# Performance work log

Hardware: AMD Instinct MI355X
Metric: run time of the kernel (lower is better)

Reference implementation:

```python
import jax, jax.numpy as jnp
import numpy as np

EPS = 1e-5
LEAKY = 0.2


def _wn(v, g):
    # weight norm over all dims except output-channel dim 0 (torch default dim=0)
    return g * v / jnp.sqrt(jnp.sum(v * v, axis=(1, 2), keepdims=True))


def _conv1d(x_bsc, w, b):
    # x_bsc: [B,S,C_in]; w: [C_out,C_in,3]; kernel 3, stride 1, pad 1
    x = x_bsc.transpose(0, 2, 1)  # NCH
    y = jax.lax.conv_general_dilated(x, w, (1,), [(1, 1)],
                                     dimension_numbers=("NCH", "OIH", "NCH"))
    y = y + b[None, :, None]
    return y.transpose(0, 2, 1)


def _adain(x, style, lengths, proj_w, proj_b):
    # masked per-(sample,channel) instance norm over valid length, then style affine, then mask
    B, S, H = x.shape
    hs = style @ proj_w.T + proj_b            # [B, 2H]
    gamma, beta = hs[:, :H], hs[:, H:]
    mask = (jnp.arange(S)[None, :] < lengths[:, None]).astype(x.dtype)[..., None]  # [B,S,1]
    cnt = lengths.astype(x.dtype)[:, None, None]
    mean = jnp.sum(x * mask, axis=1, keepdims=True) / cnt
    var = jnp.sum(jnp.square(x - mean) * mask, axis=1, keepdims=True) / cnt  # biased, as F.instance_norm
    xn = (x - mean) * jax.lax.rsqrt(var + EPS)
    out = ((1.0 + gamma[:, None, :]) * xn + beta[:, None, :]) * mask
    return out, mask


def setup_inputs() -> dict:
    key = jax.random.key(0)
    ks = jax.random.split(key, 12)
    B, S, H, STY = 8, 2048, 512, 128
    inp = {
        "hidden_states": jax.random.normal(ks[0], (B, S, H), jnp.float32),
        "style": jax.random.normal(ks[1], (B, STY), jnp.float32),
        "input_lengths": jax.random.randint(ks[2], (B,), S // 2, S + 1, jnp.int32),
        # AdaIN projections (torch Linear: [out,in])
        "proj1_w": jax.random.normal(ks[3], (2 * H, STY), jnp.float32) * 0.02,
        "proj1_b": jnp.zeros((2 * H,), jnp.float32),
        "proj2_w": jax.random.normal(ks[4], (2 * H, STY), jnp.float32) * 0.02,
        "proj2_b": jnp.zeros((2 * H,), jnp.float32),
        # weight-normed conv1 / conv2: v [out,in,3], g [out,1,1], bias [out]
        "conv1_v": jax.random.normal(ks[5], (H, H, 3), jnp.float32) * 0.02,
        "conv1_g": jnp.ones((H, 1, 1), jnp.float32),
        "conv1_b": jnp.zeros((H,), jnp.float32),
        "conv2_v": jax.random.normal(ks[6], (H, H, 3), jnp.float32) * 0.02,
        "conv2_g": jnp.ones((H, 1, 1), jnp.float32),
        "conv2_b": jnp.zeros((H,), jnp.float32),
    }
    return inp


def reference(hidden_states, style, input_lengths,
              proj1_w, proj1_b, proj2_w, proj2_b,
              conv1_v, conv1_g, conv1_b, conv2_v, conv2_g, conv2_b):
    w1 = _wn(conv1_v, conv1_g)
    w2 = _wn(conv2_v, conv2_g)
    # residual branch
    h, mask = _adain(hidden_states, style, input_lengths, proj1_w, proj1_b)
    h = jnp.where(h >= 0, h, LEAKY * h)
    h = _conv1d(h, w1, conv1_b) * mask
    h, _ = _adain(h, style, input_lengths, proj2_w, proj2_b)
    h = jnp.where(h >= 0, h, LEAKY * h)
    h = _conv1d(h, w2, conv2_b) * mask
    # shortcut is identity (no upsample, no learned shortcut)
    return (h + hidden_states) / jnp.sqrt(jnp.asarray(2.0, hidden_states.dtype))
```

## Files before the change

kernel.cpp:

```cpp
#include <hip/hip_runtime.h>

#define NB 8
#define SS 2048
#define HH 512
#define NSTY 128
#define SP (SS + 2)
#define EPSF 1e-5f

#define BM 128
#define BN 128
#define BK 64

typedef __attribute__((ext_vector_type(8))) short short8;
typedef __attribute__((ext_vector_type(4))) float floatx4;
typedef __attribute__((ext_vector_type(4))) unsigned short u16x4;
typedef unsigned short u16;

__device__ __forceinline__ float bf2f(u16 u) {
  union { float f; unsigned int i; } v; v.i = ((unsigned int)u) << 16; return v.f;
}
__device__ __forceinline__ u16 f2bf(float f) {
  union { float f; unsigned int i; } v; v.f = f;
  unsigned int x = v.i;
  return (u16)((x + 0x7fffu + ((x >> 16) & 1u)) >> 16);
}
__device__ __forceinline__ float lrelu(float v) { return v >= 0.f ? v : 0.2f * v; }

__device__ __forceinline__ void gld_lds16(const u16* g, u16* l) {
  __builtin_amdgcn_global_load_lds((const __attribute__((address_space(1))) void*)g,
                                   (__attribute__((address_space(3))) void*)l, 16, 0, 0);
}

__global__ void k_setup(const float* __restrict__ style,
                        const float* __restrict__ p1w, const float* __restrict__ p1b,
                        const float* __restrict__ p2w, const float* __restrict__ p2b,
                        const float* __restrict__ c1v, const float* __restrict__ c1g,
                        const float* __restrict__ c2v, const float* __restrict__ c2g,
                        u16* __restrict__ wt1, u16* __restrict__ wt2,
                        float* __restrict__ g1, float* __restrict__ be1,
                        float* __restrict__ g2, float* __restrict__ be2,
                        float* __restrict__ stats ) {
  int bid = blockIdx.x;
  if (bid < 2 * HH) {
    int o = bid % HH;
    int which = bid / HH;
    const float* v = which ? c2v : c1v;
    const float* g = which ? c2g : c1g;
    u16* wt = which ? wt2 : wt1;
    float s = 0.f;
    for (int e = threadIdx.x; e < HH * 3; e += 256) {
      float x = v[o * HH * 3 + e];
      s += x * x;
    }
    for (int off = 32; off > 0; off >>= 1) s += __shfl_down(s, off, 64);
    __shared__ float red[4];
    int wid = threadIdx.x >> 6, lane = threadIdx.x & 63;
    if (lane == 0) red[wid] = s;
    __syncthreads();
    float tot = red[0] + red[1] + red[2] + red[3];
    float scale = g[o] / sqrtf(tot);
    for (int e = threadIdx.x; e < HH * 3; e += 256) {
      int i = e / 3, k = e % 3;
      wt[(k * HH + o) * HH + i] = f2bf(v[o * HH * 3 + e] * scale);
    }
  } else if (bid < 2 * HH + 64) {
    int idx = (bid - 2 * HH) * 256 + threadIdx.x;
    int which = idx / (NB * 2 * HH);
    int r = idx % (NB * 2 * HH);
    int b = r / (2 * HH);
    int j = r % (2 * HH);
    const float* w = which ? p2w : p1w;
    const float* bias = which ? p2b : p1b;
    float acc = bias[j];
    const float* st = style + b * NSTY;
    const float* wr = w + j * NSTY;
    for (int t = 0; t < NSTY; t++) acc += st[t] * wr[t];
    float* gd = which ? g2 : g1;
    float* bd = which ? be2 : be1;
    if (j < HH) gd[b * HH + j] = acc;
    else        bd[b * HH + (j - HH)] = acc;
  } else {
    int i = (bid - 2 * HH - 64) * 256 + threadIdx.x;
    stats[i] = 0.f;
  }
}

#define SSPLIT1 64
__global__ void k_stats_f32(const float* __restrict__ x, const int* __restrict__ lens,
                            float* __restrict__ sum, float* __restrict__ sumsq) {
  int b = blockIdx.x & 7;
  int chunk = blockIdx.x >> 3;
  int s0 = chunk * (SS / SSPLIT1);
  int h4 = (threadIdx.x & 127) * 4;
  int sr = threadIdx.x >> 7;
  int len = lens[b];
  float4 sm = {0.f, 0.f, 0.f, 0.f}, sq = {0.f, 0.f, 0.f, 0.f};
#pragma unroll
  for (int i = 0; i < 16; i++) {
    int s = s0 + i * 2 + sr;
    float4 v = *(const float4*)(x + ((long)(b * SS + s)) * HH + h4);
    float m = (s < len) ? 1.f : 0.f;
    v.x *= m; v.y *= m; v.z *= m; v.w *= m;
    sm.x += v.x; sm.y += v.y; sm.z += v.z; sm.w += v.w;
    sq.x += v.x * v.x; sq.y += v.y * v.y; sq.z += v.z * v.z; sq.w += v.w * v.w;
  }
  atomicAdd(&sum[b * HH + h4 + 0], sm.x);
  atomicAdd(&sum[b * HH + h4 + 1], sm.y);
  atomicAdd(&sum[b * HH + h4 + 2], sm.z);
  atomicAdd(&sum[b * HH + h4 + 3], sm.w);
  atomicAdd(&sumsq[b * HH + h4 + 0], sq.x);
  atomicAdd(&sumsq[b * HH + h4 + 1], sq.y);
  atomicAdd(&sumsq[b * HH + h4 + 2], sq.z);
  atomicAdd(&sumsq[b * HH + h4 + 3], sq.w);
}

__global__ void k_prep_f32(const float* __restrict__ x,
                           const float* __restrict__ sum, const float* __restrict__ sumsq,
                           const float* __restrict__ gam, const float* __restrict__ bet,
                           const int* __restrict__ lens, u16* __restrict__ z) {
  __shared__ float a_tab[HH], c_tab[HH];
  int b = blockIdx.x & 7;
  int c = blockIdx.x >> 3;
  int len = lens[b];
  {
    float rc = 1.f / (float)len;
    int i0 = threadIdx.x * 2;
    float2 sm = *(const float2*)(sum + b * HH + i0);
    float2 sq = *(const float2*)(sumsq + b * HH + i0);
    float2 gv = *(const float2*)(gam + b * HH + i0);
    float2 bv = *(const float2*)(bet + b * HH + i0);
    float m0 = sm.x * rc, m1 = sm.y * rc;
    float a0 = (1.f + gv.x) * rsqrtf(sq.x * rc - m0 * m0 + EPSF);
    float a1 = (1.f + gv.y) * rsqrtf(sq.y * rc - m1 * m1 + EPSF);
    a_tab[i0] = a0;            a_tab[i0 + 1] = a1;
    c_tab[i0] = bv.x - m0 * a0; c_tab[i0 + 1] = bv.y - m1 * a1;
  }
  __syncthreads();
  int r = c * 2 + (threadIdx.x >> 7);
  int i = (threadIdx.x & 127) * 4;
  int s = r - 1;
  u16x4 outv;
  if (s < 0 || s >= SS || s >= len) {
    outv = (u16x4){0, 0, 0, 0};
  } else {
    const float4 xv = *(const float4*)(x + ((long)(b * SS + s)) * HH + i);
    const float4 av = *(const float4*)(&a_tab[i]);
    const float4 cv = *(const float4*)(&c_tab[i]);
    outv.x = f2bf(lrelu(av.x * xv.x + cv.x));
    outv.y = f2bf(lrelu(av.y * xv.y + cv.y));
    outv.z = f2bf(lrelu(av.z * xv.z + cv.z));
    outv.w = f2bf(lrelu(av.w * xv.w + cv.w));
  }
  *(u16x4*)(z + ((long)(b * SP + r)) * HH + i) = outv;
}

__global__ void k_prep_bf16(const u16* __restrict__ y,
                            const float* __restrict__ sum, const float* __restrict__ sumsq,
                            const float* __restrict__ gam, const float* __restrict__ bet,
                            const int* __restrict__ lens, u16* __restrict__ z) {
  __shared__ float a_tab[HH], c_tab[HH];
  int b = blockIdx.x & 7;
  int c = blockIdx.x >> 3;
  int len = lens[b];
  {
    float rc = 1.f / (float)len;
    int i0 = threadIdx.x * 2;
    float2 sm = *(const float2*)(sum + b * HH + i0);
    float2 sq = *(const float2*)(sumsq + b * HH + i0);
    float2 gv = *(const float2*)(gam + b * HH + i0);
    float2 bv = *(const float2*)(bet + b * HH + i0);
    float m0 = sm.x * rc, m1 = sm.y * rc;
    float a0 = (1.f + gv.x) * rsqrtf(sq.x * rc - m0 * m0 + EPSF);
    float a1 = (1.f + gv.y) * rsqrtf(sq.y * rc - m1 * m1 + EPSF);
    a_tab[i0] = a0;            a_tab[i0 + 1] = a1;
    c_tab[i0] = bv.x - m0 * a0; c_tab[i0 + 1] = bv.y - m1 * a1;
  }
  __syncthreads();
  int r = c * 2 + (threadIdx.x >> 7);
  int i = (threadIdx.x & 127) * 4;
  int s = r - 1;
  u16x4 outv;
  if (s < 0 || s >= SS || s >= len) {
    outv = (u16x4){0, 0, 0, 0};
  } else {
    const u16x4 yv = *(const u16x4*)(y + ((long)(b * SS + s)) * HH + i);
    const float4 av = *(const float4*)(&a_tab[i]);
    const float4 cv = *(const float4*)(&c_tab[i]);
    outv.x = f2bf(lrelu(av.x * bf2f(yv.x) + cv.x));
    outv.y = f2bf(lrelu(av.y * bf2f(yv.y) + cv.y));
    outv.z = f2bf(lrelu(av.z * bf2f(yv.z) + cv.z));
    outv.w = f2bf(lrelu(av.w * bf2f(yv.w) + cv.w));
  }
  *(u16x4*)(z + ((long)(b * SP + r)) * HH + i) = outv;
}

__global__ __launch_bounds__(512, 4) void k_conv(const u16* __restrict__ z,
                                                 const u16* __restrict__ wt,
                                                 const float* __restrict__ bias,
                                                 const int* __restrict__ lens,
                                                 u16* __restrict__ yout,
                                                 const float* __restrict__ resid,
                                                 float* __restrict__ fout,
                                                 float* __restrict__ sum,
                                                 float* __restrict__ sumsq) {
  __shared__ __align__(16) u16 L[2][2][BM * BK];

  int nwg = gridDim.x;
  int bid = blockIdx.x;
  int t = (bid & 7) * (nwg >> 3) + (bid >> 3);
  int bn0 = (t % (HH / BN)) * BN; t /= (HH / BN);
  int bm0 = (t % (SS / BM)) * BM; t /= (SS / BM);
  int b = t;

  int tid = threadIdx.x;
  int wave = tid >> 6, lane = tid & 63;
  int team = wave >> 2;
  int tw = wave & 3;
  int wr = tw >> 1, wc = tw & 1;
  int l15 = lane & 15, l4 = lane >> 4;

  int t256 = tid & 255;
  int trow = t256 >> 3;
  int tslot = t256 & 7;

  u16* LA = &L[team][0][0];
  u16* LB = &L[team][1][0];

  const u16* zb = z + (size_t)b * SP * HH;
  int len = lens[b];
  int kt0 = team * 12;

  floatx4 acc[4][4] = {};

  for (int kt = 0; kt < 12; kt++) {
    int k0 = (kt0 + kt) * BK;
    const u16* wkb = wt + (size_t)(k0 >> 9) * HH * HH + (k0 & 511);
#pragma unroll
    for (int rr = 0; rr < 4; rr++) {
      int r = rr * 32 + trow;
      int sc = (tslot ^ (r & 7)) * 8;
      gld_lds16(zb + (size_t)(bm0 + r) * HH + k0 + sc, LA + rr * 2048 + t256 * 8);
    }
#pragma unroll
    for (int rr = 0; rr < 4; rr++) {
      int r = rr * 32 + trow;
      int sc = (tslot ^ (r & 7)) * 8;
      gld_lds16(wkb + (size_t)(bn0 + r) * HH + sc, LB + rr * 2048 + t256 * 8);
    }
    __syncthreads();
#pragma unroll
    for (int kk = 0; kk < 2; kk++) {
      short8 afr[4], bfr[4];
#pragma unroll
      for (int i = 0; i < 4; i++) {
        int ar = wr * 64 + i * 16 + l15;
        afr[i] = *(const short8*)&LA[ar * BK + (((kk * 4 + l4) ^ (ar & 7)) * 8)];
      }
#pragma unroll
      for (int j = 0; j < 4; j++) {
        int br = wc * 64 + j * 16 + l15;
        bfr[j] = *(const short8*)&LB[br * BK + (((kk * 4 + l4) ^ (br & 7)) * 8)];
      }
#pragma unroll
      for (int am = 0; am < 4; am++)
#pragma unroll
        for (int bn = 0; bn < 4; bn++)
          acc[am][bn] = __builtin_amdgcn_mfma_f32_16x16x32_bf16(afr[am], bfr[bn], acc[am][bn], 0, 0, 0);
    }
    __syncthreads();
  }

  floatx4* scr = (floatx4*)&L[0][0][0];
  floatx4* my = scr + (size_t)team * 2048;
  if (team == 0) {
#pragma unroll
    for (int am = 0; am < 4; am++) {
      my[(am * 2 + 0) * 256 + t256] = acc[am][2];
      my[(am * 2 + 1) * 256 + t256] = acc[am][3];
    }
  } else {
#pragma unroll
    for (int am = 0; am < 4; am++) {
      my[(am * 2 + 0) * 256 + t256] = acc[am][0];
      my[(am * 2 + 1) * 256 + t256] = acc[am][1];
    }
  }
  __syncthreads();
  const floatx4* other = scr + (size_t)(team ^ 1) * 2048;
  if (team == 0) {
#pragma unroll
    for (int am = 0; am < 4; am++) {
      acc[am][0] += other[(am * 2 + 0) * 256 + t256];
      acc[am][1] += other[(am * 2 + 1) * 256 + t256];
    }
  } else {
#pragma unroll
    for (int am = 0; am < 4; am++) {
      acc[am][2] += other[(am * 2 + 0) * 256 + t256];
      acc[am][3] += other[(am * 2 + 1) * 256 + t256];
    }
  }

#define EPI(BN_) do {                                                        \
    int o = bn0 + wc * 64 + (BN_) * 16 + l15;                                \
    float bv = bias[o];                                                      \
    float psum = 0.f, psq = 0.f;                                             \
    _Pragma("unroll")                                                        \
    for (int am = 0; am < 4; am++) {                                         \
      _Pragma("unroll")                                                      \
      for (int r = 0; r < 4; r++) {                                          \
        int s = bm0 + wr * 64 + am * 16 + l4 * 4 + r;                        \
        float v = acc[am][BN_][r] + bv;                                      \
        v = (s < len) ? v : 0.f;                                             \
        size_t off = ((size_t)(b * SS + s)) * HH + o;                        \
        if (fout) {                                                          \
          fout[off] = (v + resid[off]) * 0.70710678118654752f;               \
        } else {                                                             \
          yout[off] = f2bf(v);                                               \
          psum += v;                                                         \
          psq += v * v;                                                      \
        }                                                                    \
      }                                                                      \
    }                                                                        \
    if (sum) {                                                               \
      psum += __shfl_xor(psum, 16, 64);                                      \
      psum += __shfl_xor(psum, 32, 64);                                      \
      psq  += __shfl_xor(psq, 16, 64);                                       \
      psq  += __shfl_xor(psq, 32, 64);                                       \
      if (l4 == 0) {                                                         \
        atomicAdd(&sum[b * HH + o], psum);                                   \
        atomicAdd(&sumsq[b * HH + o], psq);                                  \
      }                                                                      \
    }                                                                        \
  } while (0)

  if (team == 0) { EPI(0); EPI(1); }
  else           { EPI(2); EPI(3); }
#undef EPI
}

extern "C" void kernel_launch(void* const* d_in, const int* in_sizes, int n_in,
                              void* d_out, int out_size, void* d_ws, size_t ws_size,
                              hipStream_t stream) {
  const float* x    = (const float*)d_in[0];
  const float* sty  = (const float*)d_in[1];
  const int*   lens = (const int*)d_in[2];
  const float* p1w  = (const float*)d_in[3];
  const float* p1b  = (const float*)d_in[4];
  const float* p2w  = (const float*)d_in[5];
  const float* p2b  = (const float*)d_in[6];
  const float* c1v  = (const float*)d_in[7];
  const float* c1g  = (const float*)d_in[8];
  const float* c1b  = (const float*)d_in[9];
  const float* c2v  = (const float*)d_in[10];
  const float* c2g  = (const float*)d_in[11];
  const float* c2b  = (const float*)d_in[12];
  float* out = (float*)d_out;

  char* ws = (char*)d_ws;
  size_t cur = 0;
  auto alloc = [&](size_t bytes) {
    void* p = ws + cur;
    cur += (bytes + 255) & ~(size_t)255;
    return p;
  };
  u16*   wt1  = (u16*)alloc((size_t)3 * HH * HH * 2);
  u16*   wt2  = (u16*)alloc((size_t)3 * HH * HH * 2);
  float* g1   = (float*)alloc(NB * HH * 4);
  float* be1  = (float*)alloc(NB * HH * 4);
  float* g2   = (float*)alloc(NB * HH * 4);
  float* be2  = (float*)alloc(NB * HH * 4);
  float* sum1 = (float*)alloc(NB * HH * 4);
  float* sq1  = (float*)alloc(NB * HH * 4);
  float* sum2 = (float*)alloc(NB * HH * 4);
  float* sq2  = (float*)alloc(NB * HH * 4);
  u16*   z1   = (u16*)alloc((size_t)NB * SP * HH * 2);
  u16*   y1   = (u16*)alloc((size_t)NB * SS * HH * 2);
  u16*   z2   = (u16*)alloc((size_t)NB * SP * HH * 2);

  const int CGRID = NB * (SS / BM) * (HH / BN);

  k_setup<<<2 * HH + 128, 256, 0, stream>>>(sty, p1w, p1b, p2w, p2b,
                                            c1v, c1g, c2v, c2g,
                                            wt1, wt2, g1, be1, g2, be2, sum1);

  k_stats_f32<<<NB * SSPLIT1, 256, 0, stream>>>(x, lens, sum1, sq1);

  k_prep_f32<<<NB * (SP * HH / 4 / 256), 256, 0, stream>>>(x, sum1, sq1, g1, be1,
                                                           lens, z1);

  k_conv<<<CGRID, 512, 0, stream>>>(z1, wt1, c1b, lens, y1,
                                    nullptr, nullptr, sum2, sq2);

  k_prep_bf16<<<NB * (SP * HH / 4 / 256), 256, 0, stream>>>(y1, sum2, sq2, g2, be2,
                                                            lens, z2);

  k_conv<<<CGRID, 512, 0, stream>>>(z2, wt2, c2b, lens, nullptr,
                                    x, out, nullptr, nullptr);
}
```

Measured before the change: 115.3 us.

## Use producer-consumer warp specialization with double-buffered LDS in conv GEMM

Replaces the split-K scheme, where two teams of four waves each took half the K range and reduced through LDS, with warp specialization. Waves 4-7 issue global-to-LDS loads into a double buffer while waves 0-3 run MFMA on the other buffer, separated by one barrier per K tile. This removes the cross-team LDS reduction and overlaps loads with compute. The cost is that half the waves no longer do math, so per-tile MFMA throughput per block is halved.

```diff
diff --git a/kernel.cpp b/kernel.cpp
--- a/kernel.cpp
+++ b/kernel.cpp
@@ -214,52 +214,52 @@
 
   int tid = threadIdx.x;
   int wave = tid >> 6, lane = tid & 63;
-  int team = wave >> 2;
-  int tw = wave & 3;
-  int wr = tw >> 1, wc = tw & 1;
+  int wr = (wave >> 1) & 1, wc = wave & 1;
   int l15 = lane & 15, l4 = lane >> 4;
 
   int t256 = tid & 255;
   int trow = t256 >> 3;
   int tslot = t256 & 7;
 
-  u16* LA = &L[team][0][0];
-  u16* LB = &L[team][1][0];
-
   const u16* zb = z + (size_t)b * SP * HH;
   int len = lens[b];
-  int kt0 = team * 12;
 
   floatx4 acc[4][4] = {};
 
-  for (int kt = 0; kt < 12; kt++) {
-    int k0 = (kt0 + kt) * BK;
+  auto stage = [&](int buf, int kt) {
+    int k0 = kt * BK;
     const u16* wkb = wt + (size_t)(k0 >> 9) * HH * HH + (k0 & 511);
+    u16* dA = &L[buf][0][0];
+    u16* dB = &L[buf][1][0];
 #pragma unroll
     for (int rr = 0; rr < 4; rr++) {
       int r = rr * 32 + trow;
       int sc = (tslot ^ (r & 7)) * 8;
-      gld_lds16(zb + (size_t)(bm0 + r) * HH + k0 + sc, LA + rr * 2048 + t256 * 8);
+      gld_lds16(zb + (size_t)(bm0 + r) * HH + k0 + sc, dA + rr * 2048 + t256 * 8);
     }
 #pragma unroll
     for (int rr = 0; rr < 4; rr++) {
       int r = rr * 32 + trow;
       int sc = (tslot ^ (r & 7)) * 8;
-      gld_lds16(wkb + (size_t)(bn0 + r) * HH + sc, LB + rr * 2048 + t256 * 8);
-    }
-    __syncthreads();
+      gld_lds16(wkb + (size_t)(bn0 + r) * HH + sc, dB + rr * 2048 + t256 * 8);
+    }
+  };
+
+  auto compute = [&](int buf) {
+    const u16* sA = &L[buf][0][0];
+    const u16* sB = &L[buf][1][0];
 #pragma unroll
     for (int kk = 0; kk < 2; kk++) {
       short8 afr[4], bfr[4];
 #pragma unroll
       for (int i = 0; i < 4; i++) {
         int ar = wr * 64 + i * 16 + l15;
-        afr[i] = *(const short8*)&LA[ar * BK + (((kk * 4 + l4) ^ (ar & 7)) * 8)];
+        afr[i] = *(const short8*)&sA[ar * BK + (((kk * 4 + l4) ^ (ar & 7)) * 8)];
       }
 #pragma unroll
       for (int j = 0; j < 4; j++) {
         int br = wc * 64 + j * 16 + l15;
-        bfr[j] = *(const short8*)&LB[br * BK + (((kk * 4 + l4) ^ (br & 7)) * 8)];
+        bfr[j] = *(const short8*)&sB[br * BK + (((kk * 4 + l4) ^ (br & 7)) * 8)];
       }
 #pragma unroll
       for (int am = 0; am < 4; am++)
@@ -267,76 +267,56 @@
         for (int bn = 0; bn < 4; bn++)
           acc[am][bn] = __builtin_amdgcn_mfma_f32_16x16x32_bf16(afr[am], bfr[bn], acc[am][bn], 0, 0, 0);
     }
+  };
+
+  const int NT = 3 * HH / BK;
+  if (wave >= 4) stage(0, 0);
+  __syncthreads();
+
+  for (int kt = 0; kt < NT; kt++) {
+    if (wave >= 4) {
+      if (kt + 1 < NT) stage((kt + 1) & 1, kt + 1);
+    } else {
+      compute(kt & 1);
+    }
     __syncthreads();
   }
 
-  floatx4* scr = (floatx4*)&L[0][0][0];
-  floatx4* my = scr + (size_t)team * 2048;
-  if (team == 0) {
+  if (wave >= 4) return;
+
+#pragma unroll
+  for (int bn = 0; bn < 4; bn++) {
+    int o = bn0 + wc * 64 + bn * 16 + l15;
+    float bv = bias[o];
+    float psum = 0.f, psq = 0.f;
 #pragma unroll
     for (int am = 0; am < 4; am++) {
-      my[(am * 2 + 0) * 256 + t256] = acc[am][2];
-      my[(am * 2 + 1) * 256 + t256] = acc[am][3];
-    }
-  } else {
-#pragma unroll
-    for (int am = 0; am < 4; am++) {
-      my[(am * 2 + 0) * 256 + t256] = acc[am][0];
-      my[(am * 2 + 1) * 256 + t256] = acc[am][1];
-    }
-  }
-  __syncthreads();
-  const floatx4* other = scr + (size_t)(team ^ 1) * 2048;
-  if (team == 0) {
-#pragma unroll
-    for (int am = 0; am < 4; am++) {
-      acc[am][0] += other[(am * 2 + 0) * 256 + t256];
-      acc[am][1] += other[(am * 2 + 1) * 256 + t256];
-    }
-  } else {
-#pragma unroll
-    for (int am = 0; am < 4; am++) {
-      acc[am][2] += other[(am * 2 + 0) * 256 + t256];
-      acc[am][3] += other[(am * 2 + 1) * 256 + t256];
-    }
-  }
-
-#define EPI(BN_) do {                                                        \
-    int o = bn0 + wc * 64 + (BN_) * 16 + l15;                                \
-    float bv = bias[o];                                                      \
-    float psum = 0.f, psq = 0.f;                                             \
-    _Pragma("unroll")                                                        \
-    for (int am = 0; am < 4; am++) {                                         \
-      _Pragma("unroll")                                                      \
-      for (int r = 0; r < 4; r++) {                                          \
-        int s = bm0 + wr * 64 + am * 16 + l4 * 4 + r;                        \
-        float v = acc[am][BN_][r] + bv;                                      \
-        v = (s < len) ? v : 0.f;                                             \
-        size_t off = ((size_t)(b * SS + s)) * HH + o;                        \
-        if (fout) {                                                          \
-          fout[off] = (v + resid[off]) * 0.70710678118654752f;               \
-        } else {                                                             \
-          yout[off] = f2bf(v);                                               \
-          psum += v;                                                         \
-          psq += v * v;                                                      \
-        }                                                                    \
-      }                                                                      \
-    }                                                                        \
-    if (sum) {                                                               \
-      psum += __shfl_xor(psum, 16, 64);                                      \
-      psum += __shfl_xor(psum, 32, 64);                                      \
-      psq  += __shfl_xor(psq, 16, 64);                                       \
-      psq  += __shfl_xor(psq, 32, 64);                                       \
-      if (l4 == 0) {                                                         \
-        atomicAdd(&sum[b * HH + o], psum);                                   \
-        atomicAdd(&sumsq[b * HH + o], psq);                                  \
-      }                                                                      \
-    }                                                                        \
-  } while (0)
-
-  if (team == 0) { EPI(0); EPI(1); }
-  else           { EPI(2); EPI(3); }
-#undef EPI
+#pragma unroll
+      for (int r = 0; r < 4; r++) {
+        int s = bm0 + wr * 64 + am * 16 + l4 * 4 + r;
+        float v = acc[am][bn][r] + bv;
+        v = (s < len) ? v : 0.f;
+        size_t off = ((size_t)(b * SS + s)) * HH + o;
+        if (fout) {
+          fout[off] = (v + resid[off]) * 0.70710678118654752f;
+        } else {
+          yout[off] = f2bf(v);
+          psum += v;
+          psq += v * v;
+        }
+      }
+    }
+    if (sum) {
+      psum += __shfl_xor(psum, 16, 64);
+      psum += __shfl_xor(psum, 32, 64);
+      psq  += __shfl_xor(psq, 16, 64);
+      psq  += __shfl_xor(psq, 32, 64);
+      if (l4 == 0) {
+        atomicAdd(&sum[b * HH + o], psum);
+        atomicAdd(&sumsq[b * HH + o], psq);
+      }
+    }
+  }
 }
 
 extern "C" void kernel_launch(void* const* d_in, const int* in_sizes, int n_in,
```

After: 119.3 us. +3.4%, slower.
